# Kernel optimization log

Hardware: AMD Instinct MI355X
Metric: run time of the kernel (lower is better)

## Reference

```python
import jax, jax.numpy as jnp
import numpy as np

N_SIDE = 14          # ViT-S/16 on 224x224 -> 14x14 patches
D_BACKBONE = 384
D_MODEL = 512
B_CLIPS = 32
T_FRAMES = 64
BT = B_CLIPS * T_FRAMES
LN_EPS = 1e-5


def setup_inputs() -> dict:
    key = jax.random.key(0)
    k0, k1, k2, k3, k4 = jax.random.split(key, 5)
    patch_tokens = jax.random.normal(k0, (BT, N_SIDE * N_SIDE, D_BACKBONE), dtype=jnp.float32)
    raw = jax.random.uniform(k1, (BT, 4), dtype=jnp.float32)
    # make well-formed boxes: x1<=x2, y1<=y2 (module clamps anyway)
    xy1 = jnp.minimum(raw[:, :2], raw[:, 2:])
    xy2 = jnp.maximum(raw[:, :2], raw[:, 2:])
    bboxes = jnp.concatenate([xy1, xy2], axis=1)
    obj_visible = jax.random.bernoulli(k2, 0.9, (BT,)).astype(jnp.float32)
    W = jax.random.normal(k3, (D_BACKBONE, D_MODEL), dtype=jnp.float32) * 0.02
    b = jnp.zeros((D_MODEL,), dtype=jnp.float32)
    gamma = jnp.ones((D_MODEL,), dtype=jnp.float32)
    beta = jnp.zeros((D_MODEL,), dtype=jnp.float32)
    mask_token = jax.random.normal(k4, (1, D_MODEL), dtype=jnp.float32) * 0.02
    return {"patch_tokens": patch_tokens, "bboxes": bboxes, "obj_visible": obj_visible,
            "B": B_CLIPS, "T": T_FRAMES, "W": W, "b": b, "gamma": gamma, "beta": beta,
            "mask_token": mask_token}


def _roi_mean_pool(patch_tokens, bboxes):
    bt, N, D = patch_tokens.shape
    n = N_SIDE
    grid = patch_tokens.reshape(bt, n, n, D)
    # exact replica of torch index math (clamp -> trunc/ceil -> clamp -> max)
    x1 = jnp.clip(bboxes[:, 0] * n, 0, n - 1).astype(jnp.int32)
    y1 = jnp.clip(bboxes[:, 1] * n, 0, n - 1).astype(jnp.int32)
    x2 = jnp.clip(jnp.ceil(jnp.clip(bboxes[:, 2] * n, 0, n)), 1, n).astype(jnp.int32)
    y2 = jnp.clip(jnp.ceil(jnp.clip(bboxes[:, 3] * n, 0, n)), 1, n).astype(jnp.int32)
    x2 = jnp.maximum(x2, x1 + 1)
    y2 = jnp.maximum(y2, y1 + 1)
    idx = jnp.arange(n)
    my = (idx[None, :] >= y1[:, None]) & (idx[None, :] < y2[:, None])  # [BT, n]
    mx = (idx[None, :] >= x1[:, None]) & (idx[None, :] < x2[:, None])  # [BT, n]
    mask = (my[:, :, None] & mx[:, None, :]).astype(grid.dtype)        # [BT, n, n]
    count = ((y2 - y1) * (x2 - x1)).astype(grid.dtype)                 # >= 1 always
    pooled = jnp.einsum('bhw,bhwd->bd', mask, grid) / count[:, None]
    return pooled


def reference(patch_tokens, bboxes, obj_visible, B, T, W, b, gamma, beta, mask_token):
    pooled = _roi_mean_pool(patch_tokens, bboxes)          # [BT, D_backbone]
    out = pooled @ W + b                                   # [BT, d_model]
    mu = jnp.mean(out, axis=-1, keepdims=True)
    var = jnp.mean(jnp.square(out - mu), axis=-1, keepdims=True)
    out = (out - mu) * jax.lax.rsqrt(var + LN_EPS) * gamma + beta
    vis = obj_visible[:, None]
    out = vis * out + (1.0 - vis) * mask_token             # learnable mask token blend
    return out.reshape(B, T, -1)
```

## Files before the change

kernel.cpp:

```cpp
#include <hip/hip_runtime.h>
#include <hip/hip_bf16.h>

#define N_SIDE 14
#define N_PATCH (N_SIDE * N_SIDE)
#define D_BB 384
#define DQ_BB (D_BB / 4)
#define D_MODEL 512
#define BT_TOTAL 2048
#define LN_EPS 1e-5f
#define PGROUPS 8
#define KSTEPS (D_BB / 32)
#define NTILES (D_MODEL / 16)

typedef __attribute__((ext_vector_type(8))) short bf16x8;
typedef __attribute__((ext_vector_type(4))) float f32x4;

__device__ __forceinline__ unsigned short f2b(float f) {
    unsigned u = __float_as_uint(f);
    return (unsigned short)((u + 0x7FFFu + ((u >> 16) & 1u)) >> 16);
}

__device__ __forceinline__ void add4(float4& a, const float4& b) {
    a.x += b.x; a.y += b.y; a.z += b.z; a.w += b.w;
}

__device__ __forceinline__ void box_params(const float* __restrict__ bboxes, int bt,
                                           int& x1, int& y1, int& wd, int& total) {
    const float bx1 = bboxes[bt * 4 + 0];
    const float by1 = bboxes[bt * 4 + 1];
    const float bx2 = bboxes[bt * 4 + 2];
    const float by2 = bboxes[bt * 4 + 3];
    x1 = (int)fminf(fmaxf(bx1 * (float)N_SIDE, 0.f), (float)(N_SIDE - 1));
    y1 = (int)fminf(fmaxf(by1 * (float)N_SIDE, 0.f), (float)(N_SIDE - 1));
    int x2 = (int)fminf(fmaxf(ceilf(fminf(fmaxf(bx2 * (float)N_SIDE, 0.f), (float)N_SIDE)), 1.f), (float)N_SIDE);
    int y2 = (int)fminf(fmaxf(ceilf(fminf(fmaxf(by2 * (float)N_SIDE, 0.f), (float)N_SIDE)), 1.f), (float)N_SIDE);
    x2 = max(x2, x1 + 1);
    y2 = max(y2, y1 + 1);
    wd = x2 - x1;
    total = wd * (y2 - y1);
}

__global__ __launch_bounds__(768) void pool_kernel(
    const float* __restrict__ patch,
    const float* __restrict__ bboxes,
    const float* __restrict__ W,
    unsigned short* __restrict__ pooled_bf,
    unsigned short* __restrict__ wpack)
{
    const int bt = blockIdx.x;
    const int t  = threadIdx.x;
    const int qd = t % DQ_BB;
    const int g  = t / DQ_BB;

    if (bt < 64) {
        const int nt   = bt >> 1;
        const int kh   = bt & 1;
        const int lane = t & 63;
        const int grp  = t >> 6;
        const int ksl  = grp >> 1;
        const int jh   = grp & 1;
        const int ks   = kh * 6 + ksl;
        const int n    = nt * 16 + (lane & 15);
        const int kb   = ks * 32 + (lane >> 4) * 8 + jh * 4;
        ushort4 w4;
        w4.x = f2b(W[(size_t)(kb + 0) * D_MODEL + n]);
        w4.y = f2b(W[(size_t)(kb + 1) * D_MODEL + n]);
        w4.z = f2b(W[(size_t)(kb + 2) * D_MODEL + n]);
        w4.w = f2b(W[(size_t)(kb + 3) * D_MODEL + n]);
        *(ushort4*)(wpack + ((size_t)(nt * KSTEPS + ks) * 64 + lane) * 8 + jh * 4) = w4;
    }

    int x1, y1, wd, total;
    box_params(bboxes, bt, x1, y1, wd, total);
    const float inv_count = 1.f / (float)total;
    const float inv_wd = 1.f / (float)wd;
    const int cell0 = y1 * N_SIDE + x1;

    const float4* __restrict__ base = (const float4*)patch + (size_t)bt * N_PATCH * DQ_BB + qd;

    auto cell_off = [&](int c) -> size_t {
        const int y = (int)(((float)c + 0.5f) * inv_wd);
        const int x = c - y * wd;
        return (size_t)(cell0 + y * N_SIDE + x) * DQ_BB;
    };

    float4 acc = make_float4(0.f, 0.f, 0.f, 0.f);
    int c = g;
    for (; c + 3 * PGROUPS < total; c += 4 * PGROUPS) {
        const float4 v0 = base[cell_off(c)];
        const float4 v1 = base[cell_off(c + PGROUPS)];
        const float4 v2 = base[cell_off(c + 2 * PGROUPS)];
        const float4 v3 = base[cell_off(c + 3 * PGROUPS)];
        acc.x += (v0.x + v1.x) + (v2.x + v3.x);
        acc.y += (v0.y + v1.y) + (v2.y + v3.y);
        acc.z += (v0.z + v1.z) + (v2.z + v3.z);
        acc.w += (v0.w + v1.w) + (v2.w + v3.w);
    }
    for (; c < total; c += PGROUPS) {
        const float4 v = base[cell_off(c)];
        acc.x += v.x; acc.y += v.y; acc.z += v.z; acc.w += v.w;
    }

    __shared__ float4 part[PGROUPS][DQ_BB];
    part[g][qd] = acc;
    __syncthreads();

    if (t < DQ_BB) {
        float4 s = part[0][t];
#pragma unroll
        for (int p = 1; p < PGROUPS; ++p) add4(s, part[p][t]);
        ushort4 o;
        o.x = f2b(s.x * inv_count);
        o.y = f2b(s.y * inv_count);
        o.z = f2b(s.z * inv_count);
        o.w = f2b(s.w * inv_count);
        *(ushort4*)(pooled_bf + (size_t)bt * D_BB + t * 4) = o;
    }
}

__global__ __launch_bounds__(512) void mfma_ln_kernel(
    const unsigned short* __restrict__ pooled_bf,
    const unsigned short* __restrict__ wpack,
    const float* __restrict__ bias,
    const float* __restrict__ gamma,
    const float* __restrict__ beta,
    const float* __restrict__ mask_tok,
    const float* __restrict__ vis,
    float* __restrict__ out)
{
    const int tid    = threadIdx.x;
    const int ch     = tid >> 6;
    const int lane   = tid & 63;
    const int lane_m = lane & 15;
    const int lane_g = lane >> 4;
    const int mrow0  = blockIdx.x * 16;

    bf16x8 afrag[KSTEPS];
    {
        const unsigned short* Arow = pooled_bf + (size_t)(mrow0 + lane_m) * D_BB + lane_g * 8;
#pragma unroll
        for (int ks = 0; ks < KSTEPS; ++ks)
            afrag[ks] = *(const bf16x8*)(Arow + ks * 32);
    }

    f32x4 acc[4];
#pragma unroll
    for (int nt = 0; nt < 4; ++nt) acc[nt] = (f32x4){0.f, 0.f, 0.f, 0.f};

#pragma unroll
    for (int nt = 0; nt < 4; ++nt) {
        const unsigned short* bp = wpack + ((size_t)((ch * 4 + nt) * KSTEPS) * 64 + lane) * 8;
#pragma unroll
        for (int ks = 0; ks < KSTEPS; ++ks) {
            const bf16x8 b = *(const bf16x8*)(bp + (size_t)ks * 64 * 8);
            acc[nt] = __builtin_amdgcn_mfma_f32_16x16x32_bf16(afrag[ks], b, acc[nt], 0, 0, 0);
        }
    }

    float s[4] = {0.f, 0.f, 0.f, 0.f}, s2[4] = {0.f, 0.f, 0.f, 0.f};
#pragma unroll
    for (int nt = 0; nt < 4; ++nt) {
        const float bs = bias[ch * 64 + nt * 16 + lane_m];
#pragma unroll
        for (int r = 0; r < 4; ++r) {
            const float v = acc[nt][r] + bs;
            acc[nt][r] = v;
            s[r] += v; s2[r] += v * v;
        }
    }
#pragma unroll
    for (int off = 1; off < 16; off <<= 1) {
#pragma unroll
        for (int r = 0; r < 4; ++r) {
            s[r]  += __shfl_xor(s[r],  off);
            s2[r] += __shfl_xor(s2[r], off);
        }
    }

    __shared__ float lns[8][16][2];
    if (lane_m == 0) {
#pragma unroll
        for (int r = 0; r < 4; ++r) {
            lns[ch][lane_g * 4 + r][0] = s[r];
            lns[ch][lane_g * 4 + r][1] = s2[r];
        }
    }
    __syncthreads();

    float mean4[4], rstd4[4], v4[4], iv4[4];
#pragma unroll
    for (int r = 0; r < 4; ++r) {
        const int m = lane_g * 4 + r;
        float S = 0.f, S2 = 0.f;
#pragma unroll
        for (int c = 0; c < 8; ++c) { S += lns[c][m][0]; S2 += lns[c][m][1]; }
        const float mean = S * (1.f / (float)D_MODEL);
        const float var  = S2 * (1.f / (float)D_MODEL) - mean * mean;
        mean4[r] = mean;
        rstd4[r] = rsqrtf(var + LN_EPS);
        const float v = vis[mrow0 + m];
        v4[r] = v; iv4[r] = 1.f - v;
    }

#pragma unroll
    for (int nt = 0; nt < 4; ++nt) {
        const int n = ch * 64 + nt * 16 + lane_m;
        const float gm  = gamma[n];
        const float bt_ = beta[n];
        const float mt  = mask_tok[n];
#pragma unroll
        for (int r = 0; r < 4; ++r) {
            const int row = mrow0 + lane_g * 4 + r;
            const float o = v4[r] * ((acc[nt][r] - mean4[r]) * rstd4[r] * gm + bt_) + iv4[r] * mt;
            out[(size_t)row * D_MODEL + n] = o;
        }
    }
}

extern "C" void kernel_launch(void* const* d_in, const int* in_sizes, int n_in,
                              void* d_out, int out_size, void* d_ws, size_t ws_size,
                              hipStream_t stream) {
    const float* patch  = (const float*)d_in[0];
    const float* bboxes = (const float*)d_in[1];
    const float* vis    = (const float*)d_in[2];
    const float* W      = (const float*)d_in[5];
    const float* bias   = (const float*)d_in[6];
    const float* gamma  = (const float*)d_in[7];
    const float* beta   = (const float*)d_in[8];
    const float* mtok   = (const float*)d_in[9];

    unsigned short* pooled_bf = (unsigned short*)d_ws;
    unsigned short* wpack     = (unsigned short*)((char*)d_ws + (2u << 20));
    float* out = (float*)d_out;

    pool_kernel<<<BT_TOTAL, 768, 0, stream>>>(patch, bboxes, W, pooled_bf, wpack);
    mfma_ln_kernel<<<BT_TOTAL / 16, 512, 0, stream>>>(
        pooled_bf, wpack, bias, gamma, beta, mtok, vis, out);
}
```

Before: 32.05 us.

## Split ROI pooling across four blocks per frame and reduce partials in GEMM kernel

The pooling kernel now launches four 192-thread blocks per frame instead of one 768-thread block. Each block sums a strided subset of the box cells and writes fp32 partial sums to a workspace. The GEMM+LayerNorm kernel sums the four partials, divides by the cell count, converts to bf16 and stages the A tile in shared memory. This aims to improve occupancy and load balance for boxes of uneven size. In exchange it adds extra global traffic for the partials (about 12.6MB written and read) and an extra reduction step in the second kernel.

Measured after the change: 34.24 us. +6.8%, slower.

```diff
diff --git a/kernel.cpp b/kernel.cpp
--- a/kernel.cpp
+++ b/kernel.cpp
@@ -8,9 +8,11 @@
 #define D_MODEL 512
 #define BT_TOTAL 2048
 #define LN_EPS 1e-5f
-#define PGROUPS 8
 #define KSTEPS (D_BB / 32)
-#define NTILES (D_MODEL / 16)
+#define SPLIT4 4
+#define PGR 2
+#define ESTR (SPLIT4 * PGR)
+#define ALDS_P 392
 
 typedef __attribute__((ext_vector_type(8))) short bf16x8;
 typedef __attribute__((ext_vector_type(4))) float f32x4;
@@ -40,39 +42,44 @@
     total = wd * (y2 - y1);
 }
 
-__global__ __launch_bounds__(768) void pool_kernel(
+__global__ __launch_bounds__(192) void pool_kernel(
     const float* __restrict__ patch,
     const float* __restrict__ bboxes,
     const float* __restrict__ W,
-    unsigned short* __restrict__ pooled_bf,
+    float* __restrict__ part4,
     unsigned short* __restrict__ wpack)
 {
-    const int bt = blockIdx.x;
-    const int t  = threadIdx.x;
-    const int qd = t % DQ_BB;
-    const int g  = t / DQ_BB;
-
-    if (bt < 64) {
-        const int nt   = bt >> 1;
-        const int kh   = bt & 1;
+    const int bid = blockIdx.x;
+    const int bt  = bid >> 2;
+    const int q   = bid & 3;
+    const int t   = threadIdx.x;
+    const int qd  = t % DQ_BB;
+    const int g   = t / DQ_BB;
+
+    if (bid < 64) {
+        const int nt   = bid >> 1;
+        const int kh   = bid & 1;
         const int lane = t & 63;
-        const int grp  = t >> 6;
-        const int ksl  = grp >> 1;
-        const int jh   = grp & 1;
-        const int ks   = kh * 6 + ksl;
-        const int n    = nt * 16 + (lane & 15);
-        const int kb   = ks * 32 + (lane >> 4) * 8 + jh * 4;
-        ushort4 w4;
-        w4.x = f2b(W[(size_t)(kb + 0) * D_MODEL + n]);
-        w4.y = f2b(W[(size_t)(kb + 1) * D_MODEL + n]);
-        w4.z = f2b(W[(size_t)(kb + 2) * D_MODEL + n]);
-        w4.w = f2b(W[(size_t)(kb + 3) * D_MODEL + n]);
-        *(ushort4*)(wpack + ((size_t)(nt * KSTEPS + ks) * 64 + lane) * 8 + jh * 4) = w4;
+        const int w3   = t >> 6;
+#pragma unroll
+        for (int u = 0; u < 4; ++u) {
+            const int grp = w3 * 4 + u;
+            const int ksl = grp >> 1;
+            const int jh  = grp & 1;
+            const int ks  = kh * 6 + ksl;
+            const int n   = nt * 16 + (lane & 15);
+            const int kb  = ks * 32 + (lane >> 4) * 8 + jh * 4;
+            ushort4 w4;
+            w4.x = f2b(W[(size_t)(kb + 0) * D_MODEL + n]);
+            w4.y = f2b(W[(size_t)(kb + 1) * D_MODEL + n]);
+            w4.z = f2b(W[(size_t)(kb + 2) * D_MODEL + n]);
+            w4.w = f2b(W[(size_t)(kb + 3) * D_MODEL + n]);
+            *(ushort4*)(wpack + ((size_t)(nt * KSTEPS + ks) * 64 + lane) * 8 + jh * 4) = w4;
+        }
     }
 
     int x1, y1, wd, total;
     box_params(bboxes, bt, x1, y1, wd, total);
-    const float inv_count = 1.f / (float)total;
     const float inv_wd = 1.f / (float)wd;
     const int cell0 = y1 * N_SIDE + x1;
 
@@ -84,42 +91,38 @@
         return (size_t)(cell0 + y * N_SIDE + x) * DQ_BB;
     };
 
+    const int e = q * PGR + g;
     float4 acc = make_float4(0.f, 0.f, 0.f, 0.f);
-    int c = g;
-    for (; c + 3 * PGROUPS < total; c += 4 * PGROUPS) {
+    int c = e;
+    for (; c + 3 * ESTR < total; c += 4 * ESTR) {
         const float4 v0 = base[cell_off(c)];
-        const float4 v1 = base[cell_off(c + PGROUPS)];
-        const float4 v2 = base[cell_off(c + 2 * PGROUPS)];
-        const float4 v3 = base[cell_off(c + 3 * PGROUPS)];
+        const float4 v1 = base[cell_off(c + ESTR)];
+        const float4 v2 = base[cell_off(c + 2 * ESTR)];
+        const float4 v3 = base[cell_off(c + 3 * ESTR)];
         acc.x += (v0.x + v1.x) + (v2.x + v3.x);
         acc.y += (v0.y + v1.y) + (v2.y + v3.y);
         acc.z += (v0.z + v1.z) + (v2.z + v3.z);
         acc.w += (v0.w + v1.w) + (v2.w + v3.w);
     }
-    for (; c < total; c += PGROUPS) {
+    for (; c < total; c += ESTR) {
         const float4 v = base[cell_off(c)];
         acc.x += v.x; acc.y += v.y; acc.z += v.z; acc.w += v.w;
     }
 
-    __shared__ float4 part[PGROUPS][DQ_BB];
+    __shared__ float4 part[PGR][DQ_BB];
     part[g][qd] = acc;
     __syncthreads();
 
     if (t < DQ_BB) {
         float4 s = part[0][t];
-#pragma unroll
-        for (int p = 1; p < PGROUPS; ++p) add4(s, part[p][t]);
-        ushort4 o;
-        o.x = f2b(s.x * inv_count);
-        o.y = f2b(s.y * inv_count);
-        o.z = f2b(s.z * inv_count);
-        o.w = f2b(s.w * inv_count);
-        *(ushort4*)(pooled_bf + (size_t)bt * D_BB + t * 4) = o;
+        add4(s, part[1][t]);
+        ((float4*)part4)[((size_t)q * BT_TOTAL + bt) * DQ_BB + t] = s;
     }
 }
 
 __global__ __launch_bounds__(512) void mfma_ln_kernel(
-    const unsigned short* __restrict__ pooled_bf,
+    const float* __restrict__ part4,
+    const float* __restrict__ bboxes,
     const unsigned short* __restrict__ wpack,
     const float* __restrict__ bias,
     const float* __restrict__ gamma,
@@ -135,13 +138,44 @@
     const int lane_g = lane >> 4;
     const int mrow0  = blockIdx.x * 16;
 
+    __shared__ float s_invc[16];
+    __shared__ unsigned short alds[16][ALDS_P];
+    __shared__ float lns[8][16][2];
+
+    if (tid < 16) {
+        int x1, y1, wd, total;
+        box_params(bboxes, mrow0 + tid, x1, y1, wd, total);
+        s_invc[tid] = 1.f / (float)total;
+    }
+    __syncthreads();
+
+    {
+        const float4* p4 = (const float4*)part4;
+#pragma unroll
+        for (int i = 0; i < 3; ++i) {
+            const int idx = tid + i * 512;
+            const int row = idx / DQ_BB;
+            const int qc  = idx % DQ_BB;
+            const size_t base = ((size_t)mrow0 + row) * DQ_BB + qc;
+            float4 s = p4[base];
+            add4(s, p4[(size_t)1 * BT_TOTAL * DQ_BB + base]);
+            add4(s, p4[(size_t)2 * BT_TOTAL * DQ_BB + base]);
+            add4(s, p4[(size_t)3 * BT_TOTAL * DQ_BB + base]);
+            const float ic = s_invc[row];
+            ushort4 o;
+            o.x = f2b(s.x * ic);
+            o.y = f2b(s.y * ic);
+            o.z = f2b(s.z * ic);
+            o.w = f2b(s.w * ic);
+            *(ushort4*)&alds[row][qc * 4] = o;
+        }
+    }
+    __syncthreads();
+
     bf16x8 afrag[KSTEPS];
-    {
-        const unsigned short* Arow = pooled_bf + (size_t)(mrow0 + lane_m) * D_BB + lane_g * 8;
-#pragma unroll
-        for (int ks = 0; ks < KSTEPS; ++ks)
-            afrag[ks] = *(const bf16x8*)(Arow + ks * 32);
-    }
+#pragma unroll
+    for (int ks = 0; ks < KSTEPS; ++ks)
+        afrag[ks] = *(const bf16x8*)&alds[lane_m][ks * 32 + lane_g * 8];
 
     f32x4 acc[4];
 #pragma unroll
@@ -177,7 +211,6 @@
         }
     }
 
-    __shared__ float lns[8][16][2];
     if (lane_m == 0) {
 #pragma unroll
         for (int r = 0; r < 4; ++r) {
@@ -229,11 +262,11 @@
     const float* beta   = (const float*)d_in[8];
     const float* mtok   = (const float*)d_in[9];
 
-    unsigned short* pooled_bf = (unsigned short*)d_ws;
-    unsigned short* wpack     = (unsigned short*)((char*)d_ws + (2u << 20));
+    float*          part4 = (float*)d_ws;
+    unsigned short* wpack = (unsigned short*)((char*)d_ws + (13u << 20));
     float* out = (float*)d_out;
 
-    pool_kernel<<<BT_TOTAL, 768, 0, stream>>>(patch, bboxes, W, pooled_bf, wpack);
+    pool_kernel<<<BT_TOTAL * SPLIT4, 192, 0, stream>>>(patch, bboxes, W, part4, wpack);
     mfma_ln_kernel<<<BT_TOTAL / 16, 512, 0, stream>>>(
-        pooled_bf, wpack, bias, gamma, beta, mtok, vis, out);
-}
+        part4, bboxes, wpack, bias, gamma, beta, mtok, vis, out);
+}
```

## Fuse pooling and GEMM+LayerNorm into one kernel with atomic flag dependencies

Applied to the files above, without the earlier changes.

Merges the pooling kernel and the MFMA GEMM+LayerNorm kernel into a single launch. The GEMM blocks are placed after the pooling blocks and spin on agent-scope atomic counters until their 16 pooled rows and the packed weights are ready. The aim is to remove the inter-kernel gap and let GEMM work overlap the pooling tail. The cost is an extra memset launch, spin-waiting blocks that occupy CU slots, and 768-thread GEMM blocks where a third of the threads sit idle. It also relies on blocks being dispatched in order, or the waiting blocks could deadlock.

After: 97.06 us. 203% more time.

```diff
diff --git a/kernel.cpp b/kernel.cpp
--- a/kernel.cpp
+++ b/kernel.cpp
@@ -10,7 +10,7 @@
 #define LN_EPS 1e-5f
 #define PGROUPS 8
 #define KSTEPS (D_BB / 32)
-#define NTILES (D_MODEL / 16)
+#define NGEMM (BT_TOTAL / 16)
 
 typedef __attribute__((ext_vector_type(8))) short bf16x8;
 typedef __attribute__((ext_vector_type(4))) float f32x4;
@@ -40,87 +40,13 @@
     total = wd * (y2 - y1);
 }
 
-__global__ __launch_bounds__(768) void pool_kernel(
+__global__ __launch_bounds__(768) void fused_all(
     const float* __restrict__ patch,
     const float* __restrict__ bboxes,
     const float* __restrict__ W,
+    int*         __restrict__ flags,
     unsigned short* __restrict__ pooled_bf,
-    unsigned short* __restrict__ wpack)
-{
-    const int bt = blockIdx.x;
-    const int t  = threadIdx.x;
-    const int qd = t % DQ_BB;
-    const int g  = t / DQ_BB;
-
-    if (bt < 64) {
-        const int nt   = bt >> 1;
-        const int kh   = bt & 1;
-        const int lane = t & 63;
-        const int grp  = t >> 6;
-        const int ksl  = grp >> 1;
-        const int jh   = grp & 1;
-        const int ks   = kh * 6 + ksl;
-        const int n    = nt * 16 + (lane & 15);
-        const int kb   = ks * 32 + (lane >> 4) * 8 + jh * 4;
-        ushort4 w4;
-        w4.x = f2b(W[(size_t)(kb + 0) * D_MODEL + n]);
-        w4.y = f2b(W[(size_t)(kb + 1) * D_MODEL + n]);
-        w4.z = f2b(W[(size_t)(kb + 2) * D_MODEL + n]);
-        w4.w = f2b(W[(size_t)(kb + 3) * D_MODEL + n]);
-        *(ushort4*)(wpack + ((size_t)(nt * KSTEPS + ks) * 64 + lane) * 8 + jh * 4) = w4;
-    }
-
-    int x1, y1, wd, total;
-    box_params(bboxes, bt, x1, y1, wd, total);
-    const float inv_count = 1.f / (float)total;
-    const float inv_wd = 1.f / (float)wd;
-    const int cell0 = y1 * N_SIDE + x1;
-
-    const float4* __restrict__ base = (const float4*)patch + (size_t)bt * N_PATCH * DQ_BB + qd;
-
-    auto cell_off = [&](int c) -> size_t {
-        const int y = (int)(((float)c + 0.5f) * inv_wd);
-        const int x = c - y * wd;
-        return (size_t)(cell0 + y * N_SIDE + x) * DQ_BB;
-    };
-
-    float4 acc = make_float4(0.f, 0.f, 0.f, 0.f);
-    int c = g;
-    for (; c + 3 * PGROUPS < total; c += 4 * PGROUPS) {
-        const float4 v0 = base[cell_off(c)];
-        const float4 v1 = base[cell_off(c + PGROUPS)];
-        const float4 v2 = base[cell_off(c + 2 * PGROUPS)];
-        const float4 v3 = base[cell_off(c + 3 * PGROUPS)];
-        acc.x += (v0.x + v1.x) + (v2.x + v3.x);
-        acc.y += (v0.y + v1.y) + (v2.y + v3.y);
-        acc.z += (v0.z + v1.z) + (v2.z + v3.z);
-        acc.w += (v0.w + v1.w) + (v2.w + v3.w);
-    }
-    for (; c < total; c += PGROUPS) {
-        const float4 v = base[cell_off(c)];
-        acc.x += v.x; acc.y += v.y; acc.z += v.z; acc.w += v.w;
-    }
-
-    __shared__ float4 part[PGROUPS][DQ_BB];
-    part[g][qd] = acc;
-    __syncthreads();
-
-    if (t < DQ_BB) {
-        float4 s = part[0][t];
-#pragma unroll
-        for (int p = 1; p < PGROUPS; ++p) add4(s, part[p][t]);
-        ushort4 o;
-        o.x = f2b(s.x * inv_count);
-        o.y = f2b(s.y * inv_count);
-        o.z = f2b(s.z * inv_count);
-        o.w = f2b(s.w * inv_count);
-        *(ushort4*)(pooled_bf + (size_t)bt * D_BB + t * 4) = o;
-    }
-}
-
-__global__ __launch_bounds__(512) void mfma_ln_kernel(
-    const unsigned short* __restrict__ pooled_bf,
-    const unsigned short* __restrict__ wpack,
+    unsigned short* __restrict__ wpack,
     const float* __restrict__ bias,
     const float* __restrict__ gamma,
     const float* __restrict__ beta,
@@ -128,91 +54,195 @@
     const float* __restrict__ vis,
     float* __restrict__ out)
 {
-    const int tid    = threadIdx.x;
+    const int bid = blockIdx.x;
+    const int tid = threadIdx.x;
+
+    if (bid < BT_TOTAL) {
+        const int bt = bid;
+        const int t  = tid;
+        const int qd = t % DQ_BB;
+        const int g  = t / DQ_BB;
+
+        if (bt < 64) {
+            const int nt   = bt >> 1;
+            const int kh   = bt & 1;
+            const int lane = t & 63;
+            const int grp  = t >> 6;
+            const int ksl  = grp >> 1;
+            const int jh   = grp & 1;
+            const int ks   = kh * 6 + ksl;
+            const int n    = nt * 16 + (lane & 15);
+            const int kb   = ks * 32 + (lane >> 4) * 8 + jh * 4;
+            ushort4 w4;
+            w4.x = f2b(W[(size_t)(kb + 0) * D_MODEL + n]);
+            w4.y = f2b(W[(size_t)(kb + 1) * D_MODEL + n]);
+            w4.z = f2b(W[(size_t)(kb + 2) * D_MODEL + n]);
+            w4.w = f2b(W[(size_t)(kb + 3) * D_MODEL + n]);
+            *(ushort4*)(wpack + ((size_t)(nt * KSTEPS + ks) * 64 + lane) * 8 + jh * 4) = w4;
+        }
+
+        int x1, y1, wd, total;
+        box_params(bboxes, bt, x1, y1, wd, total);
+        const float inv_count = 1.f / (float)total;
+        const float inv_wd = 1.f / (float)wd;
+        const int cell0 = y1 * N_SIDE + x1;
+
+        const float4* __restrict__ base =
+            (const float4*)patch + (size_t)bt * N_PATCH * DQ_BB + qd;
+
+        auto cell_off = [&](int c) -> size_t {
+            const int y = (int)(((float)c + 0.5f) * inv_wd);
+            const int x = c - y * wd;
+            return (size_t)(cell0 + y * N_SIDE + x) * DQ_BB;
+        };
+
+        float4 acc = make_float4(0.f, 0.f, 0.f, 0.f);
+        int c = g;
+        for (; c + 3 * PGROUPS < total; c += 4 * PGROUPS) {
+            const float4 v0 = base[cell_off(c)];
+            const float4 v1 = base[cell_off(c + PGROUPS)];
+            const float4 v2 = base[cell_off(c + 2 * PGROUPS)];
+            const float4 v3 = base[cell_off(c + 3 * PGROUPS)];
+            acc.x += (v0.x + v1.x) + (v2.x + v3.x);
+            acc.y += (v0.y + v1.y) + (v2.y + v3.y);
+            acc.z += (v0.z + v1.z) + (v2.z + v3.z);
+            acc.w += (v0.w + v1.w) + (v2.w + v3.w);
+        }
+        for (; c < total; c += PGROUPS) {
+            const float4 v = base[cell_off(c)];
+            acc.x += v.x; acc.y += v.y; acc.z += v.z; acc.w += v.w;
+        }
+
+        __shared__ float4 part[PGROUPS][DQ_BB];
+        part[g][qd] = acc;
+        __syncthreads();
+
+        if (t < DQ_BB) {
+            float4 s = part[0][t];
+#pragma unroll
+            for (int p = 1; p < PGROUPS; ++p) add4(s, part[p][t]);
+            ushort4 o;
+            o.x = f2b(s.x * inv_count);
+            o.y = f2b(s.y * inv_count);
+            o.z = f2b(s.z * inv_count);
+            o.w = f2b(s.w * inv_count);
+            *(ushort4*)(pooled_bf + (size_t)bt * D_BB + t * 4) = o;
+        }
+        __syncthreads();
+
+        if (t == 0) {
+            __hip_atomic_fetch_add(&flags[1 + (bt >> 4)], 1,
+                                   __ATOMIC_RELEASE, __HIP_MEMORY_SCOPE_AGENT);
+            if (bt < 64)
+                __hip_atomic_fetch_add(&flags[0], 1,
+                                       __ATOMIC_RELEASE, __HIP_MEMORY_SCOPE_AGENT);
+        }
+        return;
+    }
+
+    const int gblk  = bid - BT_TOTAL;
+    const int mrow0 = gblk * 16;
+
+    if (tid == 0) {
+        while (__hip_atomic_load(&flags[0], __ATOMIC_ACQUIRE,
+                                 __HIP_MEMORY_SCOPE_AGENT) < 64)
+            __builtin_amdgcn_s_sleep(2);
+        while (__hip_atomic_load(&flags[1 + gblk], __ATOMIC_ACQUIRE,
+                                 __HIP_MEMORY_SCOPE_AGENT) < 16)
+            __builtin_amdgcn_s_sleep(2);
+    }
+    __syncthreads();
+
+    __shared__ float lns[8][16][2];
+
     const int ch     = tid >> 6;
     const int lane   = tid & 63;
     const int lane_m = lane & 15;
     const int lane_g = lane >> 4;
-    const int mrow0  = blockIdx.x * 16;
-
-    bf16x8 afrag[KSTEPS];
-    {
-        const unsigned short* Arow = pooled_bf + (size_t)(mrow0 + lane_m) * D_BB + lane_g * 8;
-#pragma unroll
-        for (int ks = 0; ks < KSTEPS; ++ks)
-            afrag[ks] = *(const bf16x8*)(Arow + ks * 32);
-    }
 
     f32x4 acc[4];
-#pragma unroll
-    for (int nt = 0; nt < 4; ++nt) acc[nt] = (f32x4){0.f, 0.f, 0.f, 0.f};
-
-#pragma unroll
-    for (int nt = 0; nt < 4; ++nt) {
-        const unsigned short* bp = wpack + ((size_t)((ch * 4 + nt) * KSTEPS) * 64 + lane) * 8;
-#pragma unroll
-        for (int ks = 0; ks < KSTEPS; ++ks) {
-            const bf16x8 b = *(const bf16x8*)(bp + (size_t)ks * 64 * 8);
-            acc[nt] = __builtin_amdgcn_mfma_f32_16x16x32_bf16(afrag[ks], b, acc[nt], 0, 0, 0);
-        }
-    }
-
     float s[4] = {0.f, 0.f, 0.f, 0.f}, s2[4] = {0.f, 0.f, 0.f, 0.f};
-#pragma unroll
-    for (int nt = 0; nt < 4; ++nt) {
-        const float bs = bias[ch * 64 + nt * 16 + lane_m];
+
+    if (tid < 512) {
+        bf16x8 afrag[KSTEPS];
+        {
+            const unsigned short* Arow =
+                pooled_bf + (size_t)(mrow0 + lane_m) * D_BB + lane_g * 8;
+#pragma unroll
+            for (int ks = 0; ks < KSTEPS; ++ks)
+                afrag[ks] = *(const bf16x8*)(Arow + ks * 32);
+        }
+
+#pragma unroll
+        for (int nt = 0; nt < 4; ++nt) acc[nt] = (f32x4){0.f, 0.f, 0.f, 0.f};
+
+#pragma unroll
+        for (int nt = 0; nt < 4; ++nt) {
+            const unsigned short* bp =
+                wpack + ((size_t)((ch * 4 + nt) * KSTEPS) * 64 + lane) * 8;
+#pragma unroll
+            for (int ks = 0; ks < KSTEPS; ++ks) {
+                const bf16x8 b = *(const bf16x8*)(bp + (size_t)ks * 64 * 8);
+                acc[nt] = __builtin_amdgcn_mfma_f32_16x16x32_bf16(afrag[ks], b, acc[nt], 0, 0, 0);
+            }
+        }
+
+#pragma unroll
+        for (int nt = 0; nt < 4; ++nt) {
+            const float bs = bias[ch * 64 + nt * 16 + lane_m];
+#pragma unroll
+            for (int r = 0; r < 4; ++r) {
+                const float v = acc[nt][r] + bs;
+                acc[nt][r] = v;
+                s[r] += v; s2[r] += v * v;
+            }
+        }
+#pragma unroll
+        for (int off = 1; off < 16; off <<= 1) {
+#pragma unroll
+            for (int r = 0; r < 4; ++r) {
+                s[r]  += __shfl_xor(s[r],  off);
+                s2[r] += __shfl_xor(s2[r], off);
+            }
+        }
+        if (lane_m == 0) {
+#pragma unroll
+            for (int r = 0; r < 4; ++r) {
+                lns[ch][lane_g * 4 + r][0] = s[r];
+                lns[ch][lane_g * 4 + r][1] = s2[r];
+            }
+        }
+    }
+    __syncthreads();
+
+    if (tid < 512) {
+        float mean4[4], rstd4[4], v4[4], iv4[4];
 #pragma unroll
         for (int r = 0; r < 4; ++r) {
-            const float v = acc[nt][r] + bs;
-            acc[nt][r] = v;
-            s[r] += v; s2[r] += v * v;
-        }
-    }
-#pragma unroll
-    for (int off = 1; off < 16; off <<= 1) {
-#pragma unroll
-        for (int r = 0; r < 4; ++r) {
-            s[r]  += __shfl_xor(s[r],  off);
-            s2[r] += __shfl_xor(s2[r], off);
-        }
-    }
-
-    __shared__ float lns[8][16][2];
-    if (lane_m == 0) {
-#pragma unroll
-        for (int r = 0; r < 4; ++r) {
-            lns[ch][lane_g * 4 + r][0] = s[r];
-            lns[ch][lane_g * 4 + r][1] = s2[r];
-        }
-    }
-    __syncthreads();
-
-    float mean4[4], rstd4[4], v4[4], iv4[4];
-#pragma unroll
-    for (int r = 0; r < 4; ++r) {
-        const int m = lane_g * 4 + r;
-        float S = 0.f, S2 = 0.f;
-#pragma unroll
-        for (int c = 0; c < 8; ++c) { S += lns[c][m][0]; S2 += lns[c][m][1]; }
-        const float mean = S * (1.f / (float)D_MODEL);
-        const float var  = S2 * (1.f / (float)D_MODEL) - mean * mean;
-        mean4[r] = mean;
-        rstd4[r] = rsqrtf(var + LN_EPS);
-        const float v = vis[mrow0 + m];
-        v4[r] = v; iv4[r] = 1.f - v;
-    }
-
-#pragma unroll
-    for (int nt = 0; nt < 4; ++nt) {
-        const int n = ch * 64 + nt * 16 + lane_m;
-        const float gm  = gamma[n];
-        const float bt_ = beta[n];
-        const float mt  = mask_tok[n];
-#pragma unroll
-        for (int r = 0; r < 4; ++r) {
-            const int row = mrow0 + lane_g * 4 + r;
-            const float o = v4[r] * ((acc[nt][r] - mean4[r]) * rstd4[r] * gm + bt_) + iv4[r] * mt;
-            out[(size_t)row * D_MODEL + n] = o;
+            const int m = lane_g * 4 + r;
+            float S = 0.f, S2 = 0.f;
+#pragma unroll
+            for (int cc = 0; cc < 8; ++cc) { S += lns[cc][m][0]; S2 += lns[cc][m][1]; }
+            const float mean = S * (1.f / (float)D_MODEL);
+            const float var  = S2 * (1.f / (float)D_MODEL) - mean * mean;
+            mean4[r] = mean;
+            rstd4[r] = rsqrtf(var + LN_EPS);
+            const float v = vis[mrow0 + m];
+            v4[r] = v; iv4[r] = 1.f - v;
+        }
+
+#pragma unroll
+        for (int nt = 0; nt < 4; ++nt) {
+            const int n = ch * 64 + nt * 16 + lane_m;
+            const float gm  = gamma[n];
+            const float bt_ = beta[n];
+            const float mt  = mask_tok[n];
+#pragma unroll
+            for (int r = 0; r < 4; ++r) {
+                const int row = mrow0 + lane_g * 4 + r;
+                const float o = v4[r] * ((acc[nt][r] - mean4[r]) * rstd4[r] * gm + bt_) + iv4[r] * mt;
+                out[(size_t)row * D_MODEL + n] = o;
+            }
         }
     }
 }
@@ -229,11 +259,13 @@
     const float* beta   = (const float*)d_in[8];
     const float* mtok   = (const float*)d_in[9];
 
-    unsigned short* pooled_bf = (unsigned short*)d_ws;
-    unsigned short* wpack     = (unsigned short*)((char*)d_ws + (2u << 20));
+    int*            flags     = (int*)d_ws;
+    unsigned short* pooled_bf = (unsigned short*)((char*)d_ws + (1u << 20));
+    unsigned short* wpack     = (unsigned short*)((char*)d_ws + (3u << 20));
     float* out = (float*)d_out;
 
-    pool_kernel<<<BT_TOTAL, 768, 0, stream>>>(patch, bboxes, W, pooled_bf, wpack);
-    mfma_ln_kernel<<<BT_TOTAL / 16, 512, 0, stream>>>(
-        pooled_bf, wpack, bias, gamma, beta, mtok, vis, out);
-}
+    hipMemsetAsync(flags, 0, 1024, stream);
+    fused_all<<<BT_TOTAL + NGEMM, 768, 0, stream>>>(
+        patch, bboxes, W, flags, pooled_bf, wpack,
+        bias, gamma, beta, mtok, vis, out);
+}
```
